# Kernel tuning notes

Measured on AMD Instinct MI355X. Metric: run time of the kernel, lower is better.

The kernel has to match this reference:

```python
import jax, jax.numpy as jnp
import numpy as np

SIGMA = 0.05
SIGMA2 = SIGMA * SIGMA
N_NODES = 100000
N_EDGES = 3200000


def setup_inputs() -> dict:
    key = jax.random.key(0)
    k1, k2, k3, k4 = jax.random.split(key, 4)
    source_points = jax.random.normal(k1, (N_NODES, 3), dtype=jnp.float32)
    target_points = jax.random.normal(k2, (N_NODES, 3), dtype=jnp.float32)
    edge_index = jax.random.randint(k3, (2, N_EDGES), 0, N_NODES, dtype=jnp.int64)
    edge_weights = jax.random.uniform(k4, (N_EDGES, 1), dtype=jnp.float32)
    return {"source_points": source_points, "target_points": target_points,
            "edge_index": edge_index, "edge_weights": edge_weights}


def reference(source_points, target_points, edge_index, edge_weights):
    N = source_points.shape[0]
    dst = edge_index[0]  # center point each edge contributes to
    nbr = edge_index[1]  # neighbor point index

    src_nb = source_points[nbr]            # [E,3]
    tgt_nb = target_points[nbr]            # [E,3]

    ones_e = jnp.ones((edge_index.shape[1],), dtype=source_points.dtype)
    counts = jnp.maximum(jax.ops.segment_sum(ones_e, dst, num_segments=N), 1.0)[:, None]
    src_centers = jax.ops.segment_sum(src_nb, dst, num_segments=N) / counts  # [N,3]
    tgt_centers = jax.ops.segment_sum(tgt_nb, dst, num_segments=N) / counts  # [N,3]

    src_diff = (src_nb - src_centers[dst]) * edge_weights  # [E,3]
    tgt_diff = tgt_nb - tgt_centers[dst]                   # [E,3]

    # per-edge outer product, scattered to per-point 3x3 covariances
    edge_mats = src_diff[:, :, None] * tgt_diff[:, None, :]          # [E,3,3]
    point_mats = jax.ops.segment_sum(edge_mats, dst, num_segments=N)  # [N,3,3]

    U, S, Vh = jnp.linalg.svd(point_mats)  # torch.svd's V = Vh^T, so U @ V^T == U @ Vh
    R0 = jnp.matmul(U, Vh)
    det = jnp.linalg.det(R0)
    ones_n = jnp.ones((N,), dtype=source_points.dtype)
    d_diag = jax.lax.stop_gradient(jnp.stack([ones_n, ones_n, det], axis=-1))  # [N,3]
    R = jnp.matmul(U * d_diag[:, None, :], Vh)  # U @ diag(d) @ Vh, proper rotation

    trans = tgt_centers - jnp.einsum('nij,nj->ni', R, src_centers)  # [N,3]

    # apply each neighbor's rigid transform and compute robust weights
    transformed = jnp.einsum('eij,ej->ei', R[nbr], src_nb) + trans[nbr]  # [E,3]
    d2 = jnp.sum(jnp.square(transformed - tgt_nb), axis=-1, keepdims=True)  # [E,1]
    new_edge_weights = SIGMA2 / (d2 + SIGMA2)
    return (R, trans, new_edge_weights)
```

## Files before the change

kernel.cpp:

```cpp
#include <hip/hip_runtime.h>
#include <math.h>

static constexpr float kSigma2 = 0.05f * 0.05f;
static constexpr int kCap2 = 2560;

__device__ __forceinline__ int load_idx(const void* ei, long long j, int is64) {
    if (is64) return (int)(((const long long*)ei)[j]);
    return ((const int*)ei)[j];
}

__global__ void k_detect(const int* __restrict__ ei32, int E, int* __restrict__ nz) {
    int t = threadIdx.x;
    int lim = E < 2048 ? E : 2048;
    int acc = 0;
    for (int k = t; k < lim; k += blockDim.x) acc |= ei32[2 * k + 1];
    if (acc) atomicOr(nz, 1);
}

__global__ void k_pack(const float* __restrict__ src, const float* __restrict__ tgt,
                       float4* __restrict__ pt, int N) {
    int i = blockIdx.x * blockDim.x + threadIdx.x;
    if (i >= N) return;
    pt[2 * i] = make_float4(src[3 * i + 0], src[3 * i + 1], src[3 * i + 2], 0.0f);
    pt[2 * i + 1] = make_float4(tgt[3 * i + 0], tgt[3 * i + 1], tgt[3 * i + 2], 0.0f);
}

__device__ void kabsch_from_M(const double M[3][3], double Rm[3][3]) {
    Rm[0][0] = 1; Rm[0][1] = 0; Rm[0][2] = 0;
    Rm[1][0] = 0; Rm[1][1] = 1; Rm[1][2] = 0;
    Rm[2][0] = 0; Rm[2][1] = 0; Rm[2][2] = 1;

    double frob2 = 0.0;
#pragma unroll
    for (int r = 0; r < 3; ++r)
#pragma unroll
        for (int c = 0; c < 3; ++c) frob2 += M[r][c] * M[r][c];
    if (frob2 <= 1e-80) return;

    double A[3][3];
#pragma unroll
    for (int r = 0; r < 3; ++r)
#pragma unroll
        for (int c = 0; c < 3; ++c) {
            double s = 0.0;
#pragma unroll
            for (int k = 0; k < 3; ++k) s += M[k][r] * M[k][c];
            A[r][c] = s;
        }
    double V[3][3] = {{1, 0, 0}, {0, 1, 0}, {0, 0, 1}};
    const int PL[3] = {0, 0, 1};
    const int QL[3] = {1, 2, 2};
    double thr = 1e-14 * frob2;
    for (int sweep = 0; sweep < 15; ++sweep) {
        double off = fabs(A[0][1]) + fabs(A[0][2]) + fabs(A[1][2]);
        if (off <= thr) break;
        for (int pi = 0; pi < 3; ++pi) {
            int p = PL[pi], q = QL[pi], r3 = 3 - p - q;
            double apq = A[p][q];
            if (apq == 0.0) continue;
            double theta = (A[q][q] - A[p][p]) / (2.0 * apq);
            double t = copysign(1.0, theta) / (fabs(theta) + sqrt(theta * theta + 1.0));
            double c = 1.0 / sqrt(t * t + 1.0);
            double s = t * c;
            A[p][p] -= t * apq;
            A[q][q] += t * apq;
            A[p][q] = 0.0; A[q][p] = 0.0;
            double arp = A[r3][p], arq = A[r3][q];
            A[r3][p] = c * arp - s * arq; A[p][r3] = A[r3][p];
            A[r3][q] = s * arp + c * arq; A[q][r3] = A[r3][q];
#pragma unroll
            for (int k = 0; k < 3; ++k) {
                double vp = V[k][p], vq = V[k][q];
                V[k][p] = c * vp - s * vq;
                V[k][q] = s * vp + c * vq;
            }
        }
    }
    double lam[3] = {A[0][0], A[1][1], A[2][2]};
    int id0 = 0, id1 = 1, id2 = 2, tt;
    if (lam[id0] < lam[id1]) { tt = id0; id0 = id1; id1 = tt; }
    if (lam[id0] < lam[id2]) { tt = id0; id0 = id2; id2 = tt; }
    if (lam[id1] < lam[id2]) { tt = id1; id1 = id2; id2 = tt; }
    double v1[3] = {V[0][id0], V[1][id0], V[2][id0]};
    double v2[3] = {V[0][id1], V[1][id1], V[2][id1]};
    double v3[3] = {V[0][id2], V[1][id2], V[2][id2]};

    double b1[3], b2[3];
#pragma unroll
    for (int r = 0; r < 3; ++r) {
        b1[r] = M[r][0] * v1[0] + M[r][1] * v1[1] + M[r][2] * v1[2];
        b2[r] = M[r][0] * v2[0] + M[r][1] * v2[1] + M[r][2] * v2[2];
    }
    double n1 = sqrt(b1[0] * b1[0] + b1[1] * b1[1] + b1[2] * b1[2]);
    if (n1 <= 1e-150) return;
    double u1[3] = {b1[0] / n1, b1[1] / n1, b1[2] / n1};
    double dot = u1[0] * b2[0] + u1[1] * b2[1] + u1[2] * b2[2];
    double w2[3] = {b2[0] - dot * u1[0], b2[1] - dot * u1[1], b2[2] - dot * u1[2]};
    double n2 = sqrt(w2[0] * w2[0] + w2[1] * w2[1] + w2[2] * w2[2]);
    double u2[3];
    if (n2 > n1 * 1e-12) {
        u2[0] = w2[0] / n2; u2[1] = w2[1] / n2; u2[2] = w2[2] / n2;
    } else {
        double ex0 = (fabs(u1[0]) < 0.9) ? 1.0 : 0.0;
        double ex1 = 1.0 - ex0;
        double cx = u1[1] * 0.0 - u1[2] * ex1;
        double cy = u1[2] * ex0 - u1[0] * 0.0;
        double cz = u1[0] * ex1 - u1[1] * ex0;
        double cn = sqrt(cx * cx + cy * cy + cz * cz);
        u2[0] = cx / cn; u2[1] = cy / cn; u2[2] = cz / cn;
    }
    double u3[3] = {u1[1] * u2[2] - u1[2] * u2[1],
                    u1[2] * u2[0] - u1[0] * u2[2],
                    u1[0] * u2[1] - u1[1] * u2[0]};
    double dV = v1[0] * (v2[1] * v3[2] - v2[2] * v3[1])
              - v1[1] * (v2[0] * v3[2] - v2[2] * v3[0])
              + v1[2] * (v2[0] * v3[1] - v2[1] * v3[0]);
    dV = (dV >= 0.0) ? 1.0 : -1.0;
#pragma unroll
    for (int r = 0; r < 3; ++r)
#pragma unroll
        for (int c = 0; c < 3; ++c)
            Rm[r][c] = u1[r] * v1[c] + u2[r] * v2[c] + dV * u3[r] * v3[c];
}


__global__ void __launch_bounds__(256) k_bhist(const void* __restrict__ ei,
                                               int* __restrict__ thist,
                                               int* __restrict__ ccnt,
                                               const int* __restrict__ nz,
                                               int E, int N, int nbuckets,
                                               int ntiles16, int ntiles4) {
    __shared__ int lhist[2048];
    __shared__ int ccl[4][16];
    int t = threadIdx.x;
    int lane = t & 63;
    long long tile = (long long)blockIdx.x * 16384;
    long long remll = (long long)E - tile;
    int rem = (remll < 16384) ? (int)remll : 16384;
    int is64 = (*nz == 0);
    for (int i = t; i < 2048; i += 256) lhist[i] = 0;
    if (t < 64) ((int*)ccl)[t] = 0;
    __syncthreads();
    if (rem == 16384) {
        for (int it = 0; it < 8; ++it) {
            long long base = tile + (long long)it * 2048 + (long long)t * 8;
            int d[8];
            if (is64) {
                const long long* p = (const long long*)ei + base;
#pragma unroll
                for (int k = 0; k < 4; ++k) {
                    longlong2 v = ((const longlong2*)p)[k];
                    d[2 * k] = (int)v.x;
                    d[2 * k + 1] = (int)v.y;
                }
            } else {
                const int* p = (const int*)ei + base;
                int4 a = ((const int4*)p)[0];
                int4 bb = ((const int4*)p)[1];
                d[0] = a.x; d[1] = a.y; d[2] = a.z; d[3] = a.w;
                d[4] = bb.x; d[5] = bb.y; d[6] = bb.z; d[7] = bb.w;
            }
            int sub = it >> 1;
#pragma unroll
            for (int k = 0; k < 8; ++k) {
                int dk = d[k];
                int bin = ((unsigned)dk < (unsigned)N) ? (dk >> 13) : -1;
                if (bin >= 0) atomicAdd(&lhist[dk >> 6], 1);
                unsigned long long valid = __ballot(bin >= 0);
                unsigned long long v0 = __ballot(bin & 1);
                unsigned long long v1 = __ballot(bin & 2);
                unsigned long long v2 = __ballot(bin & 4);
                unsigned long long v3 = __ballot(bin & 8);
                if (lane < 16) {
                    unsigned long long m = valid;
                    m &= (lane & 1) ? v0 : ~v0;
                    m &= (lane & 2) ? v1 : ~v1;
                    m &= (lane & 4) ? v2 : ~v2;
                    m &= (lane & 8) ? v3 : ~v3;
                    int c = __popcll(m);
                    if (c > 0) atomicAdd(&ccl[sub][lane], c);
                }
            }
        }
    } else {
        for (int idx = t; idx < rem; idx += 256) {
            int dk = load_idx(ei, tile + idx, is64);
            if ((unsigned)dk < (unsigned)N) {
                atomicAdd(&lhist[dk >> 6], 1);
                atomicAdd(&ccl[idx >> 12][dk >> 13], 1);
            }
        }
    }
    __syncthreads();
    int* row = thist + (long long)blockIdx.x * 2048;
    for (int b = t; b < 2048; b += 256) row[b] = lhist[b];
    if (t < 64) {
        int sub = t >> 4, c = t & 15;
        long long st = (long long)blockIdx.x * 4 + sub;
        if (st < ntiles4) ccnt[st * 16 + c] = ccl[sub][c];
    }
}

__global__ void __launch_bounds__(256) k_bsum(const int* __restrict__ thist,
                                              int* __restrict__ btot, int ntiles16) {
    int t = threadIdx.x;
    int bin = blockIdx.x * 16 + (t >> 4);
    int j = t & 15;
    int s = 0;
    for (int i = j; i < ntiles16; i += 16) s += thist[(long long)i * 2048 + bin];
#pragma unroll
    for (int off = 8; off >= 1; off >>= 1) s += __shfl_down(s, off, 16);
    if (j == 0) btot[bin] = s;
}

__global__ void k_scan(const int* __restrict__ btot, int* __restrict__ boff,
                       int* __restrict__ cur16, int* __restrict__ curC16, int nbuckets) {
    __shared__ int sm[2048];
    int t = threadIdx.x;
    int v0 = (t < nbuckets) ? btot[t] : 0;
    int v1 = (t + 1024 < nbuckets) ? btot[t + 1024] : 0;
    sm[t] = v0;
    sm[t + 1024] = v1;
    __syncthreads();
    for (int s = 1; s < 2048; s <<= 1) {
        int x0 = (t >= s) ? sm[t - s] : 0;
        int x1 = (t + 1024 >= s) ? sm[t + 1024 - s] : 0;
        __syncthreads();
        sm[t] += x0;
        sm[t + 1024] += x1;
        __syncthreads();
    }
    if (t < nbuckets) {
        int ex = sm[t] - v0;
        boff[t] = ex;
        cur16[t * 16] = ex;
        if ((t & 127) == 0) curC16[(t >> 7) * 16] = ex;
    }
    int t2 = t + 1024;
    if (t2 < nbuckets) {
        int ex = sm[t2] - v1;
        boff[t2] = ex;
        cur16[t2 * 16] = ex;
        if ((t2 & 127) == 0) curC16[(t2 >> 7) * 16] = ex;
    }
    if (t == nbuckets - 1) boff[nbuckets] = sm[t];
    if (t2 == nbuckets - 1) boff[nbuckets] = sm[t2];
}

__global__ void __launch_bounds__(256) k_cscan(const int* __restrict__ ccnt,
                                               const int* __restrict__ boff,
                                               int* __restrict__ cbase,
                                               int ntiles, int nbuckets, int ncoarse) {
    __shared__ int sm[256];
    int c = blockIdx.x;
    int t = threadIdx.x;
    int f = c * 128;
    if (f > nbuckets) f = nbuckets;
    int run = boff[f];
    for (int start = 0; start < ntiles; start += 256) {
        int i = start + t;
        int v = (i < ntiles) ? ccnt[(long long)i * 16 + c] : 0;
        sm[t] = v;
        __syncthreads();
        for (int s = 1; s < 256; s <<= 1) {
            int x = (t >= s) ? sm[t - s] : 0;
            __syncthreads();
            sm[t] += x;
            __syncthreads();
        }
        if (i < ntiles) cbase[(long long)i * 16 + c] = run + sm[t] - v;
        int tot = sm[255];
        __syncthreads();
        run += tot;
    }
}

__global__ void __launch_bounds__(256) k_cscatter(const void* __restrict__ ei,
                                                  const float* __restrict__ ew,
                                                  const int* __restrict__ cbase,
                                                  int2* __restrict__ sedge1,
                                                  const int* __restrict__ nz,
                                                  int E, int N, int ncoarse) {
    __shared__ int2 stage[4096];
    __shared__ unsigned char binOf[4096];
    __shared__ int hist[16];
    __shared__ int excl[16];
    __shared__ int gbase[16];
    __shared__ int woffs[4][16];
    __shared__ int wbase[4][16];
    int t = threadIdx.x;
    int w = t >> 6, lane = t & 63;
    unsigned long long lanebelow = ((unsigned long long)1 << lane) - 1;
    long long tile = (long long)blockIdx.x * 4096;
    long long remll = (long long)E - tile;
    int rem = (remll < 4096) ? (int)remll : 4096;
    int is64 = (*nz == 0);
    if (t < 16) hist[t] = 0;
    if (t < 64) ((int*)woffs)[t] = 0;
    __syncthreads();

    int mybin[16];
    int mypos[16];
    int2 mypay[16];
#pragma unroll
    for (int h = 0; h < 2; ++h) {
        int dd[8], nn[8];
        float ww[8];
        int cnt8 = 0;
        int coff = h * 2048 + t * 8;
        long long cb = tile + coff;
        if (coff + 8 <= rem) {
            if (is64) {
                const long long* pd = (const long long*)ei + cb;
                const long long* pn = (const long long*)ei + (long long)E + cb;
#pragma unroll
                for (int k = 0; k < 4; ++k) {
                    longlong2 vd = ((const longlong2*)pd)[k];
                    longlong2 vn = ((const longlong2*)pn)[k];
                    dd[2 * k] = (int)vd.x; dd[2 * k + 1] = (int)vd.y;
                    nn[2 * k] = (int)vn.x; nn[2 * k + 1] = (int)vn.y;
                }
            } else {
                const int* pd = (const int*)ei + cb;
                const int* pn = (const int*)ei + (long long)E + cb;
                int4 a = ((const int4*)pd)[0], b = ((const int4*)pd)[1];
                int4 c = ((const int4*)pn)[0], d = ((const int4*)pn)[1];
                dd[0] = a.x; dd[1] = a.y; dd[2] = a.z; dd[3] = a.w;
                dd[4] = b.x; dd[5] = b.y; dd[6] = b.z; dd[7] = b.w;
                nn[0] = c.x; nn[1] = c.y; nn[2] = c.z; nn[3] = c.w;
                nn[4] = d.x; nn[5] = d.y; nn[6] = d.z; nn[7] = d.w;
            }
            const float* pw = ew + cb;
            float4 wa = ((const float4*)pw)[0], wb = ((const float4*)pw)[1];
            ww[0] = wa.x; ww[1] = wa.y; ww[2] = wa.z; ww[3] = wa.w;
            ww[4] = wb.x; ww[5] = wb.y; ww[6] = wb.z; ww[7] = wb.w;
            cnt8 = 8;
        } else {
#pragma unroll
            for (int k = 0; k < 8; ++k) {
                if (coff + k < rem) {
                    dd[cnt8] = load_idx(ei, cb + k, is64);
                    nn[cnt8] = load_idx(ei, (long long)E + cb + k, is64);
                    ww[cnt8] = ew[cb + k];
                    ++cnt8;
                }
            }
        }
#pragma unroll
        for (int k = 0; k < 8; ++k) {
            int r = h * 8 + k;
            int bin = -1;
            if (k < cnt8) {
                int d = dd[k];
                if ((unsigned)d < (unsigned)N) {
                    int n = nn[k];
                    if ((unsigned)n >= (unsigned)N) n = N;
                    bin = d >> 13;
                    mypay[r].x = (n << 13) | (d & 8191);
                    mypay[r].y = __float_as_int(ww[k]);
                }
            }
            mybin[r] = bin;
            unsigned long long valid = __ballot(bin >= 0);
            unsigned long long v0 = __ballot(bin & 1);
            unsigned long long v1 = __ballot(bin & 2);
            unsigned long long v2 = __ballot(bin & 4);
            unsigned long long v3 = __ballot(bin & 8);
            if (bin >= 0) {
                unsigned long long m = valid;
                m &= (bin & 1) ? v0 : ~v0;
                m &= (bin & 2) ? v1 : ~v1;
                m &= (bin & 4) ? v2 : ~v2;
                m &= (bin & 8) ? v3 : ~v3;
                int rank = __popcll(m & lanebelow);
                int cnt = __popcll(m);
                int cur = woffs[w][bin];
                mypos[r] = cur + rank;
                if (rank == 0) woffs[w][bin] = cur + cnt;
            }
        }
    }
    __syncthreads();
    if (t < 64) {
        int w2 = t >> 4, b = t & 15;
        int c = woffs[w2][b];
        wbase[w2][b] = (c > 0) ? atomicAdd(&hist[b], c) : 0;
    }
    __syncthreads();
    if (t == 0) {
        int run = 0;
#pragma unroll
        for (int c = 0; c < 16; ++c) { excl[c] = run; run += hist[c]; }
    }
    __syncthreads();
#pragma unroll
    for (int r = 0; r < 16; ++r) {
        if (mybin[r] >= 0) {
            int lpos = excl[mybin[r]] + wbase[w][mybin[r]] + mypos[r];
            stage[lpos] = mypay[r];
            binOf[lpos] = (unsigned char)mybin[r];
        }
    }
    if (t < 16) gbase[t] = cbase[(long long)blockIdx.x * 16 + t];
    __syncthreads();
    int total = excl[15] + hist[15];
    for (int lpos = t; lpos < total; lpos += 256) {
        int c = binOf[lpos];
        sedge1[(long long)gbase[c] + (lpos - excl[c])] = stage[lpos];
    }
}

__global__ void __launch_bounds__(256) k_fscatter(const int2* __restrict__ sedge1,
                                                  int* __restrict__ cur16,
                                                  const int* __restrict__ boff,
                                                  int2* __restrict__ sedge2,
                                                  int E, int nbuckets, int ncoarse) {
    __shared__ int2 stage[2048];
    __shared__ unsigned short binOf[2048];
    __shared__ int lhist[1024];
    __shared__ int lincl[1024];
    __shared__ int gbase[1024];
    __shared__ int co[17];
    __shared__ int s_clo, s_W;
    int t = threadIdx.x;
    if (t <= ncoarse) {
        int f = t * 128;
        if (f > nbuckets) f = nbuckets;
        co[t] = boff[f];
    }
    __syncthreads();
    int Ev = co[ncoarse];
    long long tile = (long long)blockIdx.x * 2048;
    if (tile >= Ev) return;
    long long remll = (long long)Ev - tile;
    int rem = (remll < 2048) ? (int)remll : 2048;

    if (t == 0) {
        long long p0 = tile, p1 = tile + rem - 1;
        int c0 = 0;
        while (c0 + 1 < ncoarse && p0 >= co[c0 + 1]) ++c0;
        int c1 = c0;
        while (c1 + 1 < ncoarse && p1 >= co[c1 + 1]) ++c1;
        s_clo = c0;
        s_W = (c1 - c0 + 1) * 128;
    }
    __syncthreads();
    int clo = s_clo, W = s_W;

    int2 pay[8];
    int cnt8 = 0;
    if (rem == 2048) {
        const int4* p4 = (const int4*)(sedge1 + tile + (long long)t * 8);
#pragma unroll
        for (int k = 0; k < 4; ++k) {
            int4 v = p4[k];
            pay[2 * k].x = v.x; pay[2 * k].y = v.y;
            pay[2 * k + 1].x = v.z; pay[2 * k + 1].y = v.w;
        }
        cnt8 = 8;
    } else {
        int base = t * 8;
#pragma unroll
        for (int k = 0; k < 8; ++k) {
            int idx = base + k;
            if (idx < rem) pay[cnt8++] = sedge1[tile + idx];
        }
    }

    if (W > 1024) {
        for (int k = 0; k < cnt8; ++k) {
            long long pos = tile + t * 8 + k;
            int c = clo;
            while (c + 1 < ncoarse && pos >= co[c + 1]) ++c;
            int x1 = pay[k].x;
            unsigned nbr = ((unsigned)x1) >> 13;
            int fin = c * 128 + ((x1 & 8191) >> 6);
            int gpos = atomicAdd(&cur16[fin * 16], 1);
            int2 out;
            out.x = (int)((nbr << 6) | (unsigned)(x1 & 63));
            out.y = pay[k].y;
            sedge2[gpos] = out;
        }
        return;
    }

    for (int i = t; i < W; i += 256) lhist[i] = 0;
    __syncthreads();

    int mybin[8], myrank[8];
    int2 mypay[8];
#pragma unroll
    for (int k = 0; k < 8; ++k) {
        mybin[k] = -1;
        if (k < cnt8) {
            long long pos = tile + t * 8 + k;
            int c = clo;
            while (c + 1 < ncoarse && pos >= co[c + 1]) ++c;
            int x1 = pay[k].x;
            unsigned nbr = ((unsigned)x1) >> 13;
            int rel = (c - clo) * 128 + ((x1 & 8191) >> 6);
            mybin[k] = rel;
            myrank[k] = atomicAdd(&lhist[rel], 1);
            mypay[k].x = (int)((nbr << 6) | (unsigned)(x1 & 63));
            mypay[k].y = pay[k].y;
        }
    }
    __syncthreads();
    for (int i = t; i < W; i += 256) lincl[i] = lhist[i];
    __syncthreads();
    for (int s = 1; s < W; s <<= 1) {
        int tmp[4];
        int cj = 0;
        for (int i = t; i < W; i += 256) tmp[cj++] = (i >= s) ? lincl[i - s] : 0;
        __syncthreads();
        cj = 0;
        for (int i = t; i < W; i += 256) lincl[i] += tmp[cj++];
        __syncthreads();
    }
#pragma unroll
    for (int k = 0; k < 8; ++k) {
        if (mybin[k] >= 0) {
            int ex = lincl[mybin[k]] - lhist[mybin[k]];
            int lpos = ex + myrank[k];
            stage[lpos] = mypay[k];
            binOf[lpos] = (unsigned short)mybin[k];
        }
    }
    __syncthreads();
    for (int rel = t; rel < W; rel += 256) {
        int c = lhist[rel];
        int fin = clo * 128 + rel;
        gbase[rel] = (c > 0 && fin < nbuckets) ? atomicAdd(&cur16[fin * 16], c) : 0;
    }
    __syncthreads();
    int total = lincl[W - 1];
    for (int lpos = t; lpos < total; lpos += 256) {
        int rel = binOf[lpos];
        int ex = lincl[rel] - lhist[rel];
        sedge2[gbase[rel] + (lpos - ex)] = stage[lpos];
    }
}

__global__ void __launch_bounds__(256) k_binscatter(const void* __restrict__ ei,
                                                    const float* __restrict__ ew,
                                                    int* __restrict__ cur16,
                                                    int2* __restrict__ sedge,
                                                    const int* __restrict__ nz,
                                                    int E, int N, int nbuckets) {
    __shared__ int2 stage[2048];
    __shared__ unsigned short binOf[2048];
    __shared__ int lhist[2048];
    __shared__ int lincl[2048];
    __shared__ int gbase[2048];
    int t = threadIdx.x;
    long long tile = (long long)blockIdx.x * 2048;
    long long remll = (long long)E - tile;
    int rem = (remll < 2048) ? (int)remll : 2048;
    int is64 = (*nz == 0);
    for (int i = t; i < 2048; i += 256) lhist[i] = 0;
    __syncthreads();

    int dd[8], nn[8];
    float ww[8];
    int cnt8 = 0;
    if (rem == 2048) {
        if (is64) {
            const long long* pd = (const long long*)ei + tile + (long long)t * 8;
            const long long* pn = (const long long*)ei + (long long)E + tile + (long long)t * 8;
#pragma unroll
            for (int k = 0; k < 4; ++k) {
                longlong2 vd = ((const longlong2*)pd)[k];
                longlong2 vn = ((const longlong2*)pn)[k];
                dd[2 * k] = (int)vd.x; dd[2 * k + 1] = (int)vd.y;
                nn[2 * k] = (int)vn.x; nn[2 * k + 1] = (int)vn.y;
            }
        } else {
            const int* pd = (const int*)ei + tile + (long long)t * 8;
            const int* pn = (const int*)ei + (long long)E + tile + (long long)t * 8;
            int4 a = ((const int4*)pd)[0], b = ((const int4*)pd)[1];
            int4 c = ((const int4*)pn)[0], d = ((const int4*)pn)[1];
            dd[0] = a.x; dd[1] = a.y; dd[2] = a.z; dd[3] = a.w;
            dd[4] = b.x; dd[5] = b.y; dd[6] = b.z; dd[7] = b.w;
            nn[0] = c.x; nn[1] = c.y; nn[2] = c.z; nn[3] = c.w;
            nn[4] = d.x; nn[5] = d.y; nn[6] = d.z; nn[7] = d.w;
        }
        const float* pw = ew + tile + (long long)t * 8;
        float4 wa = ((const float4*)pw)[0], wb = ((const float4*)pw)[1];
        ww[0] = wa.x; ww[1] = wa.y; ww[2] = wa.z; ww[3] = wa.w;
        ww[4] = wb.x; ww[5] = wb.y; ww[6] = wb.z; ww[7] = wb.w;
        cnt8 = 8;
    } else {
        int base = t * 8;
#pragma unroll
        for (int k = 0; k < 8; ++k) {
            int idx = base + k;
            if (idx < rem) {
                long long e = tile + idx;
                dd[cnt8] = load_idx(ei, e, is64);
                nn[cnt8] = load_idx(ei, (long long)E + e, is64);
                ww[cnt8] = ew[e];
                ++cnt8;
            }
        }
    }

    int mybin[8];
    int myrank[8];
    int2 mypay[8];
#pragma unroll
    for (int k = 0; k < 8; ++k) {
        mybin[k] = -1;
        if (k < cnt8) {
            int d = dd[k];
            if ((unsigned)d < (unsigned)N) {
                int n = nn[k];
                if ((unsigned)n >= (unsigned)N) n = N;
                int bb = d >> 6;
                mybin[k] = bb;
                myrank[k] = atomicAdd(&lhist[bb], 1);
                mypay[k].x = (n << 6) | (d & 63);
                mypay[k].y = __float_as_int(ww[k]);
            }
        }
    }
    __syncthreads();
    for (int i = t; i < 2048; i += 256) lincl[i] = lhist[i];
    __syncthreads();
    for (int s = 1; s < 2048; s <<= 1) {
        int tmp[8];
#pragma unroll
        for (int j = 0; j < 8; ++j) {
            int i = (j << 8) + t;
            tmp[j] = (i >= s) ? lincl[i - s] : 0;
        }
        __syncthreads();
#pragma unroll
        for (int j = 0; j < 8; ++j) {
            int i = (j << 8) + t;
            lincl[i] += tmp[j];
        }
        __syncthreads();
    }
#pragma unroll
    for (int k = 0; k < 8; ++k) {
        if (mybin[k] >= 0) {
            int ex = lincl[mybin[k]] - lhist[mybin[k]];
            int lpos = ex + myrank[k];
            stage[lpos] = mypay[k];
            binOf[lpos] = (unsigned short)mybin[k];
        }
    }
    __syncthreads();
    for (int bb = t; bb < 2048; bb += 256) {
        int c = lhist[bb];
        gbase[bb] = (c > 0 && bb < nbuckets) ? atomicAdd(&cur16[bb * 16], c) : 0;
    }
    __syncthreads();
    int total = lincl[2047];
    for (int lpos = t; lpos < total; lpos += 256) {
        int bb = binOf[lpos];
        int ex = lincl[bb] - lhist[bb];
        sedge[gbase[bb] + (lpos - ex)] = stage[lpos];
    }
}

__device__ __forceinline__ void mom_acc(float v[23], float w_, float4 a, float4 bb) {
    float sx = a.x, sy = a.y, sz = a.z;
    float tx = bb.x, ty = bb.y, tz = bb.z;
    v[0] += 1.0f;
    v[1] += sx; v[2] += sy; v[3] += sz;
    v[4] += tx; v[5] += ty; v[6] += tz;
    v[7] += w_;
    float wsx = w_ * sx, wsy = w_ * sy, wsz = w_ * sz;
    v[8] += wsx; v[9] += wsy; v[10] += wsz;
    v[11] += w_ * tx; v[12] += w_ * ty; v[13] += w_ * tz;
    v[14] += wsx * tx; v[15] += wsx * ty; v[16] += wsx * tz;
    v[17] += wsy * tx; v[18] += wsy * ty; v[19] += wsy * tz;
    v[20] += wsz * tx; v[21] += wsz * ty; v[22] += wsz * tz;
}

__global__ void __launch_bounds__(256) k_sortmoment(const int* __restrict__ boff,
                                                    const int2* __restrict__ sedge2,
                                                    const float4* __restrict__ pt,
                                                    float* __restrict__ momG, int N) {
    __shared__ int2 sorted[kCap2];
    __shared__ int hist[64];
    __shared__ int offs[64];
    __shared__ int scanbuf[64];
    __shared__ int woffs[4][64];
    __shared__ int wbase[4][64];
    int b = blockIdx.x, t = threadIdx.x;
    int w = t >> 6, lane = t & 63;
    unsigned long long lanebelow = ((unsigned long long)1 << lane) - 1;
    int e0 = boff[b], e1 = boff[b + 1];
    int cnt = e1 - e0;
    int inlds = (cnt <= kCap2);
    if (t < 64) hist[t] = 0;
    ((int*)woffs)[t] = 0;
    __syncthreads();
    if (inlds) {
        int2 pay[10];
        int mypos[10];
#pragma unroll
        for (int r = 0; r < 10; ++r) {
            int idx = r * 256 + t;
            int bin = -1;
            if (idx < cnt) {
                pay[r] = sedge2[e0 + idx];
                bin = pay[r].x & 63;
            }
            unsigned long long vm = __ballot(bin >= 0);
            unsigned long long b0 = __ballot(bin & 1);
            unsigned long long b1 = __ballot(bin & 2);
            unsigned long long b2 = __ballot(bin & 4);
            unsigned long long b3 = __ballot(bin & 8);
            unsigned long long b4 = __ballot(bin & 16);
            unsigned long long b5 = __ballot(bin & 32);
            if (bin >= 0) {
                unsigned long long m = vm;
                m &= (bin & 1) ? b0 : ~b0;
                m &= (bin & 2) ? b1 : ~b1;
                m &= (bin & 4) ? b2 : ~b2;
                m &= (bin & 8) ? b3 : ~b3;
                m &= (bin & 16) ? b4 : ~b4;
                m &= (bin & 32) ? b5 : ~b5;
                int rank = __popcll(m & lanebelow);
                int cm = __popcll(m);
                int curv = woffs[w][bin];
                mypos[r] = curv + rank;
                if (rank == 0) woffs[w][bin] = curv + cm;
            }
        }
        __syncthreads();
        {
            int w2 = t >> 6, bb = t & 63;
            int c = woffs[w2][bb];
            wbase[w2][bb] = (c > 0) ? atomicAdd(&hist[bb], c) : 0;
        }
        __syncthreads();
        if (t < 64) scanbuf[t] = hist[t];
        __syncthreads();
        for (int s = 1; s < 64; s <<= 1) {
            int v = 0;
            if (t < 64 && t >= s) v = scanbuf[t - s];
            __syncthreads();
            if (t < 64) scanbuf[t] += v;
            __syncthreads();
        }
        if (t < 64) offs[t] = scanbuf[t] - hist[t];
        __syncthreads();
#pragma unroll
        for (int r = 0; r < 10; ++r) {
            int idx = r * 256 + t;
            if (idx < cnt) {
                int bin = pay[r].x & 63;
                sorted[offs[bin] + wbase[w][bin] + mypos[r]] = pay[r];
            }
        }
        __syncthreads();
    }
    int oct = t >> 3, lane8 = t & 7;
#pragma unroll
    for (int rr = 0; rr < 2; ++rr) {
        int nl = oct + rr * 32;
        long long node = (long long)b * 64 + nl;
        float v[23];
#pragma unroll
        for (int i = 0; i < 23; ++i) v[i] = 0.0f;
        if (node < N) {
            if (inlds) {
                int start = offs[nl];
                int cn = hist[nl];
                int j = lane8;
                for (; j + 8 < cn; j += 16) {
                    int2 p1 = sorted[start + j];
                    int2 p2 = sorted[start + j + 8];
                    unsigned n1 = ((unsigned)p1.x) >> 6;
                    unsigned n2 = ((unsigned)p2.x) >> 6;
                    float4 a1 = pt[2 * n1], b1v = pt[2 * n1 + 1];
                    float4 a2 = pt[2 * n2], b2v = pt[2 * n2 + 1];
                    if (n1 < (unsigned)N) mom_acc(v, __int_as_float(p1.y), a1, b1v);
                    if (n2 < (unsigned)N) mom_acc(v, __int_as_float(p2.y), a2, b2v);
                }
                if (j < cn) {
                    int2 p = sorted[start + j];
                    unsigned n = ((unsigned)p.x) >> 6;
                    float4 a = pt[2 * n], bb = pt[2 * n + 1];
                    if (n < (unsigned)N) mom_acc(v, __int_as_float(p.y), a, bb);
                }
            } else {
                for (int j = lane8; j < cnt; j += 8) {
                    int2 p = sedge2[e0 + j];
                    if ((p.x & 63) != nl) continue;
                    unsigned n = ((unsigned)p.x) >> 6;
                    if (n >= (unsigned)N) continue;
                    float4 a = pt[2 * n], bb = pt[2 * n + 1];
                    mom_acc(v, __int_as_float(p.y), a, bb);
                }
            }
        }
#pragma unroll
        for (int m = 1; m < 8; m <<= 1) {
#pragma unroll
            for (int i = 0; i < 23; ++i) v[i] += __shfl_xor(v[i], m, 64);
        }
        if (lane8 == 0 && node < N) {
#pragma unroll
            for (int i = 0; i < 23; ++i) momG[(size_t)i * N + node] = v[i];
        }
    }
}

__global__ void __launch_bounds__(256) k_kabsch2(const float* __restrict__ momG,
                                                 const float4* __restrict__ pt,
                                                 float* __restrict__ Rout,
                                                 float* __restrict__ Tout,
                                                 float* __restrict__ wnode, int N) {
    int i = blockIdx.x * blockDim.x + threadIdx.x;
    if (i >= N) return;
    float m[23];
#pragma unroll
    for (int k = 0; k < 23; ++k) m[k] = momG[(size_t)k * N + i];
    double cntv = (double)m[0];
    double inv = 1.0 / fmax(cntv, 1.0);
    double sb[3] = {m[1] * inv, m[2] * inv, m[3] * inv};
    double tb[3] = {m[4] * inv, m[5] * inv, m[6] * inv};
    double Sw = m[7];
    double Sws[3] = {m[8], m[9], m[10]};
    double Swt[3] = {m[11], m[12], m[13]};
    double M[3][3];
#pragma unroll
    for (int r = 0; r < 3; ++r)
#pragma unroll
        for (int c = 0; c < 3; ++c)
            M[r][c] = (double)m[14 + 3 * r + c]
                    - sb[r] * Swt[c] - Sws[r] * tb[c] + Sw * sb[r] * tb[c];
    double Rm[3][3];
    kabsch_from_M(M, Rm);
    double T0 = tb[0] - (Rm[0][0] * sb[0] + Rm[0][1] * sb[1] + Rm[0][2] * sb[2]);
    double T1 = tb[1] - (Rm[1][0] * sb[0] + Rm[1][1] * sb[1] + Rm[1][2] * sb[2]);
    double T2 = tb[2] - (Rm[2][0] * sb[0] + Rm[2][1] * sb[1] + Rm[2][2] * sb[2]);
#pragma unroll
    for (int r = 0; r < 3; ++r)
#pragma unroll
        for (int c = 0; c < 3; ++c)
            Rout[9 * (long long)i + 3 * r + c] = (float)Rm[r][c];
    Tout[3 * i + 0] = (float)T0;
    Tout[3 * i + 1] = (float)T1;
    Tout[3 * i + 2] = (float)T2;
    float4 a = pt[2 * i];
    float4 q = pt[2 * i + 1];
    double x0 = Rm[0][0] * a.x + Rm[0][1] * a.y + Rm[0][2] * a.z + T0;
    double x1 = Rm[1][0] * a.x + Rm[1][1] * a.y + Rm[1][2] * a.z + T1;
    double x2 = Rm[2][0] * a.x + Rm[2][1] * a.y + Rm[2][2] * a.z + T2;
    double d0 = x0 - q.x, d1 = x1 - q.y, d2 = x2 - q.z;
    double dd = d0 * d0 + d1 * d1 + d2 * d2;
    wnode[i] = (float)((double)kSigma2 / (dd + (double)kSigma2));
}

__global__ void __launch_bounds__(256) k_wgather(const void* __restrict__ ei,
                                                 const float* __restrict__ wnode,
                                                 float* __restrict__ wout,
                                                 const int* __restrict__ nz,
                                                 int E, int N) {
    int gid = blockIdx.x * blockDim.x + threadIdx.x;
    long long base = (long long)gid * 8;
    if (base >= E) return;
    int is64 = (*nz == 0);
    int n_[8];
    int full = (base + 8 <= (long long)E);
    if (full) {
        if (is64) {
            const long long* p = (const long long*)ei + (long long)E + base;
#pragma unroll
            for (int k = 0; k < 4; ++k) {
                longlong2 a = ((const longlong2*)p)[k];
                n_[2 * k] = (int)a.x;
                n_[2 * k + 1] = (int)a.y;
            }
        } else {
            const int* p = (const int*)ei + (long long)E + base;
            int4 a = ((const int4*)p)[0];
            int4 b = ((const int4*)p)[1];
            n_[0] = a.x; n_[1] = a.y; n_[2] = a.z; n_[3] = a.w;
            n_[4] = b.x; n_[5] = b.y; n_[6] = b.z; n_[7] = b.w;
        }
        float w[8];
#pragma unroll
        for (int k = 0; k < 8; ++k)
            w[k] = ((unsigned)n_[k] < (unsigned)N) ? wnode[n_[k]] : 1.0f;
        *(float4*)(wout + base) = make_float4(w[0], w[1], w[2], w[3]);
        *(float4*)(wout + base + 4) = make_float4(w[4], w[5], w[6], w[7]);
    } else {
#pragma unroll
        for (int k = 0; k < 8; ++k) {
            long long e = base + k;
            if (e < E) {
                int n = load_idx(ei, (long long)E + e, is64);
                wout[e] = ((unsigned)n < (unsigned)N) ? wnode[n] : 1.0f;
            }
        }
    }
}


__global__ void k_accum1(const void* __restrict__ ei, const float* __restrict__ src,
                         const float* __restrict__ tgt, float* __restrict__ cnt,
                         float* __restrict__ ssum, float* __restrict__ tsum,
                         const int* __restrict__ nz, int E, int N) {
    int e = blockIdx.x * blockDim.x + threadIdx.x;
    if (e >= E) return;
    int is64 = (*nz == 0);
    int d = load_idx(ei, e, is64);
    int n = load_idx(ei, (long long)E + e, is64);
    if ((unsigned)d >= (unsigned)N || (unsigned)n >= (unsigned)N) return;
    atomicAdd(&cnt[d], 1.0f);
    atomicAdd(&ssum[3 * d + 0], src[3 * n + 0]);
    atomicAdd(&ssum[3 * d + 1], src[3 * n + 1]);
    atomicAdd(&ssum[3 * d + 2], src[3 * n + 2]);
    atomicAdd(&tsum[3 * d + 0], tgt[3 * n + 0]);
    atomicAdd(&tsum[3 * d + 1], tgt[3 * n + 1]);
    atomicAdd(&tsum[3 * d + 2], tgt[3 * n + 2]);
}

__global__ void k_centers(float* __restrict__ cnt, float* __restrict__ ssum,
                          float* __restrict__ tsum, int N) {
    int i = blockIdx.x * blockDim.x + threadIdx.x;
    if (i >= N) return;
    float inv = 1.0f / fmaxf(cnt[i], 1.0f);
    ssum[3 * i + 0] *= inv; ssum[3 * i + 1] *= inv; ssum[3 * i + 2] *= inv;
    tsum[3 * i + 0] *= inv; tsum[3 * i + 1] *= inv; tsum[3 * i + 2] *= inv;
}

__global__ void k_accum2(const void* __restrict__ ei, const float* __restrict__ src,
                         const float* __restrict__ tgt, const float* __restrict__ ew,
                         const float* __restrict__ sc, const float* __restrict__ tc,
                         float* __restrict__ Mm, const int* __restrict__ nz, int E, int N) {
    int e = blockIdx.x * blockDim.x + threadIdx.x;
    if (e >= E) return;
    int is64 = (*nz == 0);
    int d = load_idx(ei, e, is64);
    int n = load_idx(ei, (long long)E + e, is64);
    if ((unsigned)d >= (unsigned)N || (unsigned)n >= (unsigned)N) return;
    float w = ew[e];
    float a0 = (src[3 * n + 0] - sc[3 * d + 0]) * w;
    float a1 = (src[3 * n + 1] - sc[3 * d + 1]) * w;
    float a2 = (src[3 * n + 2] - sc[3 * d + 2]) * w;
    float b0 = tgt[3 * n + 0] - tc[3 * d + 0];
    float b1 = tgt[3 * n + 1] - tc[3 * d + 1];
    float b2 = tgt[3 * n + 2] - tc[3 * d + 2];
    float* Md = Mm + 9 * (long long)d;
    atomicAdd(Md + 0, a0 * b0); atomicAdd(Md + 1, a0 * b1); atomicAdd(Md + 2, a0 * b2);
    atomicAdd(Md + 3, a1 * b0); atomicAdd(Md + 4, a1 * b1); atomicAdd(Md + 5, a1 * b2);
    atomicAdd(Md + 6, a2 * b0); atomicAdd(Md + 7, a2 * b1); atomicAdd(Md + 8, a2 * b2);
}

__global__ void k_kabsch(const float* __restrict__ Mm, const float* __restrict__ sc,
                         const float* __restrict__ tc, float* __restrict__ Rout,
                         float* __restrict__ Tout, int N) {
    int i = blockIdx.x * blockDim.x + threadIdx.x;
    if (i >= N) return;
    double M[3][3];
#pragma unroll
    for (int r = 0; r < 3; ++r)
#pragma unroll
        for (int c = 0; c < 3; ++c)
            M[r][c] = (double)Mm[9 * (long long)i + 3 * r + c];
    double Rm[3][3];
    kabsch_from_M(M, Rm);
    double s0 = sc[3 * i + 0], s1 = sc[3 * i + 1], s2 = sc[3 * i + 2];
    double t0 = tc[3 * i + 0], t1 = tc[3 * i + 1], t2 = tc[3 * i + 2];
#pragma unroll
    for (int r = 0; r < 3; ++r)
#pragma unroll
        for (int c = 0; c < 3; ++c)
            Rout[9 * (long long)i + 3 * r + c] = (float)Rm[r][c];
    Tout[3 * i + 0] = (float)(t0 - (Rm[0][0] * s0 + Rm[0][1] * s1 + Rm[0][2] * s2));
    Tout[3 * i + 1] = (float)(t1 - (Rm[1][0] * s0 + Rm[1][1] * s1 + Rm[1][2] * s2));
    Tout[3 * i + 2] = (float)(t2 - (Rm[2][0] * s0 + Rm[2][1] * s1 + Rm[2][2] * s2));
}

__global__ void k_weights_plain(const void* __restrict__ ei,
                                const float* __restrict__ src,
                                const float* __restrict__ tgt,
                                const float* __restrict__ R,
                                const float* __restrict__ T,
                                float* __restrict__ wout,
                                const int* __restrict__ nz, int E, int N) {
    int e = blockIdx.x * blockDim.x + threadIdx.x;
    if (e >= E) return;
    int is64 = (*nz == 0);
    int n = load_idx(ei, (long long)E + e, is64);
    float w = 1.0f;
    if ((unsigned)n < (unsigned)N) {
        float p0 = src[3 * n + 0], p1 = src[3 * n + 1], p2 = src[3 * n + 2];
        float q0 = tgt[3 * n + 0], q1 = tgt[3 * n + 1], q2 = tgt[3 * n + 2];
        const float* Rn = R + 9 * (long long)n;
        const float* Tn = T + 3 * (long long)n;
        float x0 = Rn[0] * p0 + Rn[1] * p1 + Rn[2] * p2 + Tn[0];
        float x1 = Rn[3] * p0 + Rn[4] * p1 + Rn[5] * p2 + Tn[1];
        float x2 = Rn[6] * p0 + Rn[7] * p1 + Rn[8] * p2 + Tn[2];
        float d0 = x0 - q0, d1 = x1 - q1, d2 = x2 - q2;
        float dd = d0 * d0 + d1 * d1 + d2 * d2;
        w = kSigma2 / (dd + kSigma2);
    }
    wout[e] = w;
}

extern "C" void kernel_launch(void* const* d_in, const int* in_sizes, int n_in,
                              void* d_out, int out_size, void* d_ws, size_t ws_size,
                              hipStream_t stream) {
    const float* src = (const float*)d_in[0];
    const float* tgt = (const float*)d_in[1];
    const void* ei = d_in[2];
    const float* ew = (const float*)d_in[3];
    int N = in_sizes[0] / 3;
    int E = in_sizes[3];

    float* out = (float*)d_out;
    float* Rout = out;
    float* Tout = out + (size_t)9 * N;
    float* Wout = out + (size_t)12 * N;

    int eb = (E + 255) / 256;
    int nb = (N + 255) / 256;
    int nbuckets = (N + 63) / 64;
    int ncoarse = (nbuckets + 127) / 128;
    int tiles = (int)(((long long)E + 2047) / 2048);
    int ntiles4 = (int)(((long long)E + 4095) / 4096);
    int ntiles16 = (int)(((long long)E + 16383) / 16384);
    int wb8 = (int)(((long long)E + 2047) / 2048);

    size_t ctrl_ints = 16 + 2048 + (size_t)nbuckets * 16 + 256
                     + (size_t)(nbuckets + 1) + (size_t)ntiles4 * 16 * 2
                     + (size_t)ntiles16 * 2048;
    ctrl_ints = (ctrl_ints + 3) & ~(size_t)3;
    size_t after1 = ctrl_ints + 2 * (size_t)E;
    after1 = (after1 + 3) & ~(size_t)3;
    size_t after2 = after1 + 2 * (size_t)E;
    after2 = (after2 + 3) & ~(size_t)3;
    size_t tail_ints = 8 * (size_t)(N + 1) + (size_t)N + 23 * (size_t)N;
    size_t needA = (after2 + tail_ints) * sizeof(int);
    size_t needB = (after1 + tail_ints) * sizeof(int);

    if (N <= 131072 && nbuckets <= 2048 && ws_size >= needB) {
        int twolevel = (ws_size >= needA) ? 1 : 0;
        int* nz = (int*)d_ws;
        int* btot = nz + 16;
        int* cur16 = btot + 2048;
        int* curC16 = cur16 + (size_t)nbuckets * 16;
        int* boff = curC16 + 256;
        int* ccnt = boff + (nbuckets + 1);
        int* cbase = ccnt + (size_t)ntiles4 * 16;
        int* thist = cbase + (size_t)ntiles4 * 16;
        int2* sedge1 = (int2*)((int*)d_ws + ctrl_ints);
        size_t tail_base = twolevel ? after2 : after1;
        int2* sedge2 = twolevel ? (int2*)((int*)d_ws + after1) : sedge1;
        float4* pt = (float4*)((int*)d_ws + tail_base);
        float* wnode = (float*)(pt + 2 * (size_t)(N + 1));
        float* momG = wnode + N;

        hipMemsetAsync(d_ws, 0, 16 * sizeof(int), stream);

        k_detect<<<1, 256, 0, stream>>>((const int*)ei, E, nz);
        k_pack<<<nb, 256, 0, stream>>>(src, tgt, pt, N);
        k_bhist<<<ntiles16, 256, 0, stream>>>(ei, thist, ccnt, nz, E, N, nbuckets,
                                              ntiles16, ntiles4);
        k_bsum<<<128, 256, 0, stream>>>(thist, btot, ntiles16);
        k_scan<<<1, 1024, 0, stream>>>(btot, boff, cur16, curC16, nbuckets);
        if (twolevel) {
            k_cscan<<<16, 256, 0, stream>>>(ccnt, boff, cbase, ntiles4, nbuckets, ncoarse);
            k_cscatter<<<ntiles4, 256, 0, stream>>>(ei, ew, cbase, sedge1, nz, E, N, ncoarse);
            k_fscatter<<<tiles, 256, 0, stream>>>(sedge1, cur16, boff, sedge2, E, nbuckets, ncoarse);
        } else {
            k_binscatter<<<tiles, 256, 0, stream>>>(ei, ew, cur16, sedge2, nz, E, N, nbuckets);
        }
        k_sortmoment<<<nbuckets, 256, 0, stream>>>(boff, sedge2, pt, momG, N);
        k_kabsch2<<<nb, 256, 0, stream>>>(momG, pt, Rout, Tout, wnode, N);
        k_wgather<<<wb8, 256, 0, stream>>>(ei, wnode, Wout, nz, E, N);
    } else {
        float* cnt = (float*)d_ws;
        float* ssum = cnt + N;
        float* tsum = ssum + 3 * (size_t)N;
        float* Mm = tsum + 3 * (size_t)N;
        int* nz = (int*)(Mm + 9 * (size_t)N);
        size_t ws_bytes = (size_t)16 * N * sizeof(float) + 16;
        hipMemsetAsync(d_ws, 0, ws_bytes, stream);
        k_detect<<<1, 256, 0, stream>>>((const int*)ei, E, nz);
        k_accum1<<<eb, 256, 0, stream>>>(ei, src, tgt, cnt, ssum, tsum, nz, E, N);
        k_centers<<<nb, 256, 0, stream>>>(cnt, ssum, tsum, N);
        k_accum2<<<eb, 256, 0, stream>>>(ei, src, tgt, ew, ssum, tsum, Mm, nz, E, N);
        k_kabsch<<<nb, 256, 0, stream>>>(Mm, ssum, tsum, Rout, Tout, N);
        k_weights_plain<<<eb, 256, 0, stream>>>(ei, src, tgt, Rout, Tout, Wout, nz, E, N);
    }
}
```

Before: 232.1 us.

## Retile histogram and fine scatter to 4096-edge tiles with warp-ballot ranking

The bucket-histogram kernel now uses 4096-edge tiles, one per block. It derives the coarse per-tile counts by summing its fine histogram, which removes the per-element ballot counting. The fine scatter moves to 4096-edge tiles and ranks edges within each warp using ballots instead of shared-memory atomics. It falls back to direct global atomics when a tile spans more than two coarse bins. The moment kernel's gather loop is unrolled to four outstanding loads to raise memory-level parallelism. Costs are a 4x larger per-tile histogram buffer for k_bsum to reduce and more register pressure.

Measured after the change: 226.4 us. 1.03x faster.

```diff
diff --git a/kernel.cpp b/kernel.cpp
--- a/kernel.cpp
+++ b/kernel.cpp
@@ -129,20 +129,17 @@
                                                int* __restrict__ ccnt,
                                                const int* __restrict__ nz,
                                                int E, int N, int nbuckets,
-                                               int ntiles16, int ntiles4) {
+                                               int ntiles4) {
     __shared__ int lhist[2048];
-    __shared__ int ccl[4][16];
     int t = threadIdx.x;
-    int lane = t & 63;
-    long long tile = (long long)blockIdx.x * 16384;
+    long long tile = (long long)blockIdx.x * 4096;
     long long remll = (long long)E - tile;
-    int rem = (remll < 16384) ? (int)remll : 16384;
+    int rem = (remll < 4096) ? (int)remll : 4096;
     int is64 = (*nz == 0);
     for (int i = t; i < 2048; i += 256) lhist[i] = 0;
-    if (t < 64) ((int*)ccl)[t] = 0;
-    __syncthreads();
-    if (rem == 16384) {
-        for (int it = 0; it < 8; ++it) {
+    __syncthreads();
+    if (rem == 4096) {
+        for (int it = 0; it < 2; ++it) {
             long long base = tile + (long long)it * 2048 + (long long)t * 8;
             int d[8];
             if (is64) {
@@ -160,54 +157,34 @@
                 d[0] = a.x; d[1] = a.y; d[2] = a.z; d[3] = a.w;
                 d[4] = bb.x; d[5] = bb.y; d[6] = bb.z; d[7] = bb.w;
             }
-            int sub = it >> 1;
-#pragma unroll
-            for (int k = 0; k < 8; ++k) {
-                int dk = d[k];
-                int bin = ((unsigned)dk < (unsigned)N) ? (dk >> 13) : -1;
-                if (bin >= 0) atomicAdd(&lhist[dk >> 6], 1);
-                unsigned long long valid = __ballot(bin >= 0);
-                unsigned long long v0 = __ballot(bin & 1);
-                unsigned long long v1 = __ballot(bin & 2);
-                unsigned long long v2 = __ballot(bin & 4);
-                unsigned long long v3 = __ballot(bin & 8);
-                if (lane < 16) {
-                    unsigned long long m = valid;
-                    m &= (lane & 1) ? v0 : ~v0;
-                    m &= (lane & 2) ? v1 : ~v1;
-                    m &= (lane & 4) ? v2 : ~v2;
-                    m &= (lane & 8) ? v3 : ~v3;
-                    int c = __popcll(m);
-                    if (c > 0) atomicAdd(&ccl[sub][lane], c);
-                }
-            }
+#pragma unroll
+            for (int k = 0; k < 8; ++k)
+                if ((unsigned)d[k] < (unsigned)N) atomicAdd(&lhist[d[k] >> 6], 1);
         }
     } else {
         for (int idx = t; idx < rem; idx += 256) {
             int dk = load_idx(ei, tile + idx, is64);
-            if ((unsigned)dk < (unsigned)N) {
-                atomicAdd(&lhist[dk >> 6], 1);
-                atomicAdd(&ccl[idx >> 12][dk >> 13], 1);
-            }
+            if ((unsigned)dk < (unsigned)N) atomicAdd(&lhist[dk >> 6], 1);
         }
     }
     __syncthreads();
     int* row = thist + (long long)blockIdx.x * 2048;
     for (int b = t; b < 2048; b += 256) row[b] = lhist[b];
-    if (t < 64) {
-        int sub = t >> 4, c = t & 15;
-        long long st = (long long)blockIdx.x * 4 + sub;
-        if (st < ntiles4) ccnt[st * 16 + c] = ccl[sub][c];
-    }
+    int part = 0;
+#pragma unroll
+    for (int j = 0; j < 8; ++j) part += lhist[t * 8 + j];
+#pragma unroll
+    for (int off = 8; off >= 1; off >>= 1) part += __shfl_down(part, off, 16);
+    if ((t & 15) == 0) ccnt[(long long)blockIdx.x * 16 + (t >> 4)] = part;
 }
 
 __global__ void __launch_bounds__(256) k_bsum(const int* __restrict__ thist,
-                                              int* __restrict__ btot, int ntiles16) {
+                                              int* __restrict__ btot, int ntiles) {
     int t = threadIdx.x;
     int bin = blockIdx.x * 16 + (t >> 4);
     int j = t & 15;
     int s = 0;
-    for (int i = j; i < ntiles16; i += 16) s += thist[(long long)i * 2048 + bin];
+    for (int i = j; i < ntiles; i += 16) s += thist[(long long)i * 2048 + bin];
 #pragma unroll
     for (int off = 8; off >= 1; off >>= 1) s += __shfl_down(s, off, 16);
     if (j == 0) btot[bin] = s;
@@ -415,14 +392,18 @@
                                                   const int* __restrict__ boff,
                                                   int2* __restrict__ sedge2,
                                                   int E, int nbuckets, int ncoarse) {
-    __shared__ int2 stage[2048];
-    __shared__ unsigned short binOf[2048];
-    __shared__ int lhist[1024];
-    __shared__ int lincl[1024];
-    __shared__ int gbase[1024];
+    __shared__ int2 stage[4096];
+    __shared__ unsigned short binOf[4096];
+    __shared__ int hist[256];
+    __shared__ int lincl[256];
+    __shared__ int gbase[256];
+    __shared__ int woffs[4][256];
+    __shared__ int wbase[4][256];
     __shared__ int co[17];
     __shared__ int s_clo, s_W;
     int t = threadIdx.x;
+    int w = t >> 6, lane = t & 63;
+    unsigned long long lanebelow = ((unsigned long long)1 << lane) - 1;
     if (t <= ncoarse) {
         int f = t * 128;
         if (f > nbuckets) f = nbuckets;
@@ -430,10 +411,10 @@
     }
     __syncthreads();
     int Ev = co[ncoarse];
-    long long tile = (long long)blockIdx.x * 2048;
+    long long tile = (long long)blockIdx.x * 4096;
     if (tile >= Ev) return;
     long long remll = (long long)Ev - tile;
-    int rem = (remll < 2048) ? (int)remll : 2048;
+    int rem = (remll < 4096) ? (int)remll : 4096;
 
     if (t == 0) {
         long long p0 = tile, p1 = tile + rem - 1;
@@ -444,99 +425,142 @@
         s_clo = c0;
         s_W = (c1 - c0 + 1) * 128;
     }
+    hist[t] = 0;
+    for (int i = t; i < 1024; i += 256) ((int*)woffs)[i] = 0;
     __syncthreads();
     int clo = s_clo, W = s_W;
 
-    int2 pay[8];
-    int cnt8 = 0;
-    if (rem == 2048) {
-        const int4* p4 = (const int4*)(sedge1 + tile + (long long)t * 8);
-#pragma unroll
-        for (int k = 0; k < 4; ++k) {
-            int4 v = p4[k];
-            pay[2 * k].x = v.x; pay[2 * k].y = v.y;
-            pay[2 * k + 1].x = v.z; pay[2 * k + 1].y = v.w;
-        }
-        cnt8 = 8;
-    } else {
-        int base = t * 8;
+    int2 pay[16];
+#pragma unroll
+    for (int h = 0; h < 2; ++h) {
+        int coff = h * 2048 + t * 8;
+        if (coff + 8 <= rem) {
+            const int4* p4 = (const int4*)(sedge1 + tile + coff);
+#pragma unroll
+            for (int k = 0; k < 4; ++k) {
+                int4 v = p4[k];
+                pay[h * 8 + 2 * k].x = v.x;     pay[h * 8 + 2 * k].y = v.y;
+                pay[h * 8 + 2 * k + 1].x = v.z; pay[h * 8 + 2 * k + 1].y = v.w;
+            }
+        } else {
+#pragma unroll
+            for (int k = 0; k < 8; ++k)
+                if (coff + k < rem) pay[h * 8 + k] = sedge1[tile + coff + k];
+        }
+    }
+
+    if (W > 256) {
+#pragma unroll
+        for (int h = 0; h < 2; ++h) {
+#pragma unroll
+            for (int k = 0; k < 8; ++k) {
+                int coff = h * 2048 + t * 8 + k;
+                if (coff < rem) {
+                    long long pos = tile + coff;
+                    int x1 = pay[h * 8 + k].x;
+                    int c = clo;
+                    while (c + 1 < ncoarse && pos >= co[c + 1]) ++c;
+                    unsigned nbr = ((unsigned)x1) >> 13;
+                    int fin = c * 128 + ((x1 & 8191) >> 6);
+                    int gpos = atomicAdd(&cur16[fin * 16], 1);
+                    int2 out;
+                    out.x = (int)((nbr << 6) | (unsigned)(x1 & 63));
+                    out.y = pay[h * 8 + k].y;
+                    sedge2[gpos] = out;
+                }
+            }
+        }
+        return;
+    }
+
+    int mybin[16];
+    int mypos[16];
+#pragma unroll
+    for (int h = 0; h < 2; ++h) {
 #pragma unroll
         for (int k = 0; k < 8; ++k) {
-            int idx = base + k;
-            if (idx < rem) pay[cnt8++] = sedge1[tile + idx];
-        }
-    }
-
-    if (W > 1024) {
-        for (int k = 0; k < cnt8; ++k) {
-            long long pos = tile + t * 8 + k;
-            int c = clo;
-            while (c + 1 < ncoarse && pos >= co[c + 1]) ++c;
-            int x1 = pay[k].x;
+            int r = h * 8 + k;
+            int coff = h * 2048 + t * 8 + k;
+            int bin = -1;
+            if (coff < rem) {
+                long long pos = tile + coff;
+                int x1 = pay[r].x;
+                int c = clo;
+                while (c + 1 < ncoarse && pos >= co[c + 1]) ++c;
+                bin = (c - clo) * 128 + ((x1 & 8191) >> 6);
+            }
+            mybin[r] = bin;
+            unsigned long long vm = __ballot(bin >= 0);
+            unsigned long long b0 = __ballot(bin & 1);
+            unsigned long long b1 = __ballot(bin & 2);
+            unsigned long long b2 = __ballot(bin & 4);
+            unsigned long long b3 = __ballot(bin & 8);
+            unsigned long long b4 = __ballot(bin & 16);
+            unsigned long long b5 = __ballot(bin & 32);
+            unsigned long long b6 = __ballot(bin & 64);
+            unsigned long long b7 = __ballot(bin & 128);
+            if (bin >= 0) {
+                unsigned long long m = vm;
+                m &= (bin & 1) ? b0 : ~b0;
+                m &= (bin & 2) ? b1 : ~b1;
+                m &= (bin & 4) ? b2 : ~b2;
+                m &= (bin & 8) ? b3 : ~b3;
+                m &= (bin & 16) ? b4 : ~b4;
+                m &= (bin & 32) ? b5 : ~b5;
+                m &= (bin & 64) ? b6 : ~b6;
+                m &= (bin & 128) ? b7 : ~b7;
+                int rank = __popcll(m & lanebelow);
+                int cnt = __popcll(m);
+                int cur = woffs[w][bin];
+                mypos[r] = cur + rank;
+                if (rank == 0) woffs[w][bin] = cur + cnt;
+            }
+        }
+    }
+    __syncthreads();
+    {
+        int c0 = woffs[0][t], c1 = woffs[1][t], c2 = woffs[2][t], c3 = woffs[3][t];
+        int run = 0;
+        wbase[0][t] = run; run += c0;
+        wbase[1][t] = run; run += c1;
+        wbase[2][t] = run; run += c2;
+        wbase[3][t] = run; run += c3;
+        hist[t] = run;
+    }
+    __syncthreads();
+    lincl[t] = hist[t];
+    __syncthreads();
+    for (int s = 1; s < 256; s <<= 1) {
+        int x = (t >= s) ? lincl[t - s] : 0;
+        __syncthreads();
+        lincl[t] += x;
+        __syncthreads();
+    }
+#pragma unroll
+    for (int r = 0; r < 16; ++r) {
+        if (mybin[r] >= 0) {
+            int bin = mybin[r];
+            int ex = lincl[bin] - hist[bin];
+            int lpos = ex + wbase[w][bin] + mypos[r];
+            int x1 = pay[r].x;
             unsigned nbr = ((unsigned)x1) >> 13;
-            int fin = c * 128 + ((x1 & 8191) >> 6);
-            int gpos = atomicAdd(&cur16[fin * 16], 1);
             int2 out;
             out.x = (int)((nbr << 6) | (unsigned)(x1 & 63));
-            out.y = pay[k].y;
-            sedge2[gpos] = out;
-        }
-        return;
-    }
-
-    for (int i = t; i < W; i += 256) lhist[i] = 0;
-    __syncthreads();
-
-    int mybin[8], myrank[8];
-    int2 mypay[8];
-#pragma unroll
-    for (int k = 0; k < 8; ++k) {
-        mybin[k] = -1;
-        if (k < cnt8) {
-            long long pos = tile + t * 8 + k;
-            int c = clo;
-            while (c + 1 < ncoarse && pos >= co[c + 1]) ++c;
-            int x1 = pay[k].x;
-            unsigned nbr = ((unsigned)x1) >> 13;
-            int rel = (c - clo) * 128 + ((x1 & 8191) >> 6);
-            mybin[k] = rel;
-            myrank[k] = atomicAdd(&lhist[rel], 1);
-            mypay[k].x = (int)((nbr << 6) | (unsigned)(x1 & 63));
-            mypay[k].y = pay[k].y;
-        }
-    }
-    __syncthreads();
-    for (int i = t; i < W; i += 256) lincl[i] = lhist[i];
-    __syncthreads();
-    for (int s = 1; s < W; s <<= 1) {
-        int tmp[4];
-        int cj = 0;
-        for (int i = t; i < W; i += 256) tmp[cj++] = (i >= s) ? lincl[i - s] : 0;
-        __syncthreads();
-        cj = 0;
-        for (int i = t; i < W; i += 256) lincl[i] += tmp[cj++];
-        __syncthreads();
-    }
-#pragma unroll
-    for (int k = 0; k < 8; ++k) {
-        if (mybin[k] >= 0) {
-            int ex = lincl[mybin[k]] - lhist[mybin[k]];
-            int lpos = ex + myrank[k];
-            stage[lpos] = mypay[k];
-            binOf[lpos] = (unsigned short)mybin[k];
-        }
-    }
-    __syncthreads();
-    for (int rel = t; rel < W; rel += 256) {
-        int c = lhist[rel];
-        int fin = clo * 128 + rel;
-        gbase[rel] = (c > 0 && fin < nbuckets) ? atomicAdd(&cur16[fin * 16], c) : 0;
-    }
-    __syncthreads();
-    int total = lincl[W - 1];
+            out.y = pay[r].y;
+            stage[lpos] = out;
+            binOf[lpos] = (unsigned short)bin;
+        }
+    }
+    {
+        int c = hist[t];
+        int fin = clo * 128 + t;
+        gbase[t] = (c > 0 && fin < nbuckets) ? atomicAdd(&cur16[fin * 16], c) : 0;
+    }
+    __syncthreads();
+    int total = lincl[255];
     for (int lpos = t; lpos < total; lpos += 256) {
         int rel = binOf[lpos];
-        int ex = lincl[rel] - lhist[rel];
+        int ex = lincl[rel] - hist[rel];
         sedge2[gbase[rel] + (lpos - ex)] = stage[lpos];
     }
 }
@@ -772,15 +796,33 @@
                 int start = offs[nl];
                 int cn = hist[nl];
                 int j = lane8;
-                for (; j + 8 < cn; j += 16) {
-                    int2 p1 = sorted[start + j];
-                    int2 p2 = sorted[start + j + 8];
+                for (; j + 24 < cn; j += 32) {
+                    int2 p0 = sorted[start + j];
+                    int2 p1 = sorted[start + j + 8];
+                    int2 p2 = sorted[start + j + 16];
+                    int2 p3 = sorted[start + j + 24];
+                    unsigned n0 = ((unsigned)p0.x) >> 6;
                     unsigned n1 = ((unsigned)p1.x) >> 6;
                     unsigned n2 = ((unsigned)p2.x) >> 6;
+                    unsigned n3 = ((unsigned)p3.x) >> 6;
+                    float4 a0 = pt[2 * n0], b0v = pt[2 * n0 + 1];
                     float4 a1 = pt[2 * n1], b1v = pt[2 * n1 + 1];
                     float4 a2 = pt[2 * n2], b2v = pt[2 * n2 + 1];
+                    float4 a3 = pt[2 * n3], b3v = pt[2 * n3 + 1];
+                    if (n0 < (unsigned)N) mom_acc(v, __int_as_float(p0.y), a0, b0v);
                     if (n1 < (unsigned)N) mom_acc(v, __int_as_float(p1.y), a1, b1v);
                     if (n2 < (unsigned)N) mom_acc(v, __int_as_float(p2.y), a2, b2v);
+                    if (n3 < (unsigned)N) mom_acc(v, __int_as_float(p3.y), a3, b3v);
+                }
+                for (; j + 8 < cn; j += 16) {
+                    int2 p0 = sorted[start + j];
+                    int2 p1 = sorted[start + j + 8];
+                    unsigned n0 = ((unsigned)p0.x) >> 6;
+                    unsigned n1 = ((unsigned)p1.x) >> 6;
+                    float4 a0 = pt[2 * n0], b0v = pt[2 * n0 + 1];
+                    float4 a1 = pt[2 * n1], b1v = pt[2 * n1 + 1];
+                    if (n0 < (unsigned)N) mom_acc(v, __int_as_float(p0.y), a0, b0v);
+                    if (n1 < (unsigned)N) mom_acc(v, __int_as_float(p1.y), a1, b1v);
                 }
                 if (j < cn) {
                     int2 p = sorted[start + j];
@@ -1028,12 +1070,11 @@
     int ncoarse = (nbuckets + 127) / 128;
     int tiles = (int)(((long long)E + 2047) / 2048);
     int ntiles4 = (int)(((long long)E + 4095) / 4096);
-    int ntiles16 = (int)(((long long)E + 16383) / 16384);
     int wb8 = (int)(((long long)E + 2047) / 2048);
 
     size_t ctrl_ints = 16 + 2048 + (size_t)nbuckets * 16 + 256
                      + (size_t)(nbuckets + 1) + (size_t)ntiles4 * 16 * 2
-                     + (size_t)ntiles16 * 2048;
+                     + (size_t)ntiles4 * 2048;
     ctrl_ints = (ctrl_ints + 3) & ~(size_t)3;
     size_t after1 = ctrl_ints + 2 * (size_t)E;
     after1 = (after1 + 3) & ~(size_t)3;
@@ -1064,14 +1105,13 @@
 
         k_detect<<<1, 256, 0, stream>>>((const int*)ei, E, nz);
         k_pack<<<nb, 256, 0, stream>>>(src, tgt, pt, N);
-        k_bhist<<<ntiles16, 256, 0, stream>>>(ei, thist, ccnt, nz, E, N, nbuckets,
-                                              ntiles16, ntiles4);
-        k_bsum<<<128, 256, 0, stream>>>(thist, btot, ntiles16);
+        k_bhist<<<ntiles4, 256, 0, stream>>>(ei, thist, ccnt, nz, E, N, nbuckets, ntiles4);
+        k_bsum<<<128, 256, 0, stream>>>(thist, btot, ntiles4);
         k_scan<<<1, 1024, 0, stream>>>(btot, boff, cur16, curC16, nbuckets);
         if (twolevel) {
             k_cscan<<<16, 256, 0, stream>>>(ccnt, boff, cbase, ntiles4, nbuckets, ncoarse);
             k_cscatter<<<ntiles4, 256, 0, stream>>>(ei, ew, cbase, sedge1, nz, E, N, ncoarse);
-            k_fscatter<<<tiles, 256, 0, stream>>>(sedge1, cur16, boff, sedge2, E, nbuckets, ncoarse);
+            k_fscatter<<<ntiles4, 256, 0, stream>>>(sedge1, cur16, boff, sedge2, E, nbuckets, ncoarse);
         } else {
             k_binscatter<<<tiles, 256, 0, stream>>>(ei, ew, cur16, sedge2, nz, E, N, nbuckets);
         }
```
